# Performance work log

Hardware: AMD Instinct MI355X
Metric: run time of the kernel (lower is better)

## Reference

```python
import jax, jax.numpy as jnp
import numpy as np

NUM = 8          # group_heads
ALPHA = 1000.0   # Pos_Enc alpha
BETA = 100.0     # Pos_Enc beta


def setup_inputs() -> dict:
    key = jax.random.key(0)
    ks = jax.random.split(key, 19)
    N, C, H = 16384, 64, 1024
    gs1 = H // NUM
    s = 0.02
    r = lambda k, shp: jax.random.normal(k, shp, dtype=jnp.float32) * s
    return {
        "features": jax.random.normal(ks[0], (N, C), dtype=jnp.float32),
        "fc1_w": r(ks[1], (C, H)), "fc1_b": r(ks[2], (H,)),
        "fc2_w": r(ks[3], (H, C)), "fc2_b": r(ks[4], (C,)),
        "g1_w": r(ks[5], (H, H)), "g1_b": r(ks[6], (H,)),
        "g2_w": r(ks[7], (H, H)), "g2_b": r(ks[8], (H,)),
        "gg1_w": r(ks[9], (gs1, gs1)), "gg1_b": r(ks[10], (gs1,)),
        "gg2_w": r(ks[11], (gs1, gs1)), "gg2_b": r(ks[12], (gs1,)),
        "wq": r(ks[13], (H, H)), "wk": r(ks[14], (H, H)), "wv": r(ks[15], (H, H)),
        "wq2": r(ks[16], (gs1, gs1)), "wk2": r(ks[17], (gs1, gs1)),
        "lpe": jax.random.normal(ks[18], (1,), dtype=jnp.float32) * 0.1,
    }


def _mlp(x, w1, b1, w2, b2):
    return jax.nn.relu(x @ w1 + b1) @ w2 + b2


def reference(features, fc1_w, fc1_b, fc2_w, fc2_b, g1_w, g1_b, g2_w, g2_b,
              gg1_w, gg1_b, gg2_w, gg2_b, wq, wk, wv, wq2, wk2, lpe):
    N, C = features.shape
    H = fc1_w.shape[1]
    gs1 = H // NUM   # feature-group size
    gs2 = N // NUM   # token-group size

    x = features @ fc1_w + fc1_b                      # (N, H)

    # --- attn1: per-feature-group vector attention (shared weights -> vectorized)
    xg = x.reshape(N, NUM, gs1)                       # contiguous feature slices
    q1 = xg @ wq2
    k1 = xg @ wk2
    h1 = _mlp(q1 - k1, gg1_w, gg1_b, gg2_w, gg2_b)
    attn1 = jax.nn.softmax(h1 / np.sqrt(gs1).astype(np.float32), axis=0)
    attn1 = attn1.reshape(N, H)                       # concat over groups = reshape

    # --- attn2: source bug: loop uses stale i=NUM-1, so the LAST token group
    # is processed NUM times and tiled along tokens.
    gf2 = x[(NUM - 1) * gs2:, :]                      # (gs2, H)
    q2 = gf2 @ wq
    k2 = gf2 @ wk
    h2 = _mlp(q2 - k2, g1_w, g1_b, g2_w, g2_b)
    a2 = jax.nn.softmax(h2 / np.sqrt(H).astype(np.float32), axis=0)
    attn2 = jnp.tile(a2, (NUM, 1))                    # (N, H)

    attn = attn1 + attn2
    v = x @ wv                                        # (N, H)

    # --- sinusoidal positional encoding (Pos_Enc), only coord-0 slice survives
    xyz = features[:, :3]                             # (N, 3)
    feat_dim = H // 2
    feat_range = jnp.arange(feat_dim, dtype=jnp.float32)
    dim_embed = jnp.power(jnp.float32(ALPHA), feat_range / feat_dim)
    div = BETA * xyz[..., None] / dim_embed           # (N, 3, feat_dim)
    emb = jnp.concatenate([jnp.sin(div), jnp.cos(div)], axis=-1)  # (N, 3, H)
    pe = (emb + lpe[0]) * lpe[0]
    pe0 = pe[:, 0, :]                                 # (N, H) first coordinate

    res = attn * (v + pe0)                            # elementwise einsum bmf,bmf->bmf
    out = res @ fc2_w + fc2_b + features              # residual
    return out
```

## Files before the change

### kernel.cpp

```cpp
#include <hip/hip_runtime.h>
#include <hip/hip_bf16.h>
#include <math.h>
#include <type_traits>


typedef __attribute__((ext_vector_type(8))) short short8;
typedef __attribute__((ext_vector_type(4))) float f32x4;
typedef __attribute__((ext_vector_type(4))) float float4v;

#define GLOAD_LDS16(gptr, lptr)                                                 \
    __builtin_amdgcn_global_load_lds(                                           \
        (const __attribute__((address_space(1))) void*)(gptr),                  \
        (__attribute__((address_space(3))) void*)(lptr), 16, 0, 0)

static __device__ __forceinline__ unsigned short f2bf_bits(float v) {
    __hip_bfloat16 h = __float2bfloat16(v);
    return __builtin_bit_cast(unsigned short, h);
}
static __device__ __forceinline__ float bf_bits2f(unsigned short u) {
    return __bfloat162float(__builtin_bit_cast(__hip_bfloat16, u));
}
static __device__ __forceinline__ int swz16(int r, int c16) {
    return (r << 4) + (c16 ^ (r & 7));
}
static __device__ __forceinline__ int swz_elem(int r, int c) {
    return (r << 7) + ((((c << 1) ^ ((r & 7) << 4))) >> 1);
}
static __device__ __forceinline__ int xcd_swz(int bid, int nwg) {
    return (bid & 7) * (nwg >> 3) + (bid >> 3);
}

static __device__ void conv_t_dev(const float* __restrict__ A, const float* __restrict__ Bsub,
                                  __hip_bfloat16* __restrict__ Ot, int K, int N,
                                  int bx, int by, int tid, float* t )
{
    const int n0 = bx * 32, k0 = by * 32;
    const int tx = tid & 31, ty = tid >> 5;
    #pragma unroll
    for (int j = 0; j < 4; ++j) {
        int k = k0 + ty + j * 8;
        float v = A[(long)k * N + n0 + tx];
        if (Bsub) v -= Bsub[(long)k * N + n0 + tx];
        t[(ty + j * 8) * 33 + tx] = v;
    }
    __syncthreads();
    #pragma unroll
    for (int j = 0; j < 4; ++j) {
        int n = n0 + ty + j * 8;
        Ot[(long)n * K + k0 + tx] = __float2bfloat16(t[tx * 33 + ty + j * 8]);
    }
}

__global__ __launch_bounds__(256) void prep_k(
    const float* __restrict__ features, const float* __restrict__ fc1_w,
    const float* __restrict__ fc2_w, const float* __restrict__ fc2_b,
    const float* __restrict__ g1_w, const float* __restrict__ g2_w,
    const float* __restrict__ wq, const float* __restrict__ wk,
    const float* __restrict__ wv, const float* __restrict__ wq2,
    const float* __restrict__ wk2, const float* __restrict__ gg1_w,
    const float* __restrict__ gg2_w,
    __hip_bfloat16* __restrict__ featb, __hip_bfloat16* __restrict__ fc1T,
    __hip_bfloat16* __restrict__ fc2T, __hip_bfloat16* __restrict__ wdT,
    __hip_bfloat16* __restrict__ wvT, __hip_bfloat16* __restrict__ g1T,
    __hip_bfloat16* __restrict__ g2T, __hip_bfloat16* __restrict__ wd2T,
    __hip_bfloat16* __restrict__ gg1T, __hip_bfloat16* __restrict__ gg2T,
    float* __restrict__ invde, float* __restrict__ out)
{
    __shared__ float t[32 * 33];
    const int bid = blockIdx.x;
    const int tid = threadIdx.x;

    if (bid == 0) {
        #pragma unroll
        for (int i = 0; i < 2; ++i) {
            int idx = tid + i * 256;
            invde[idx] = exp2f(-9.96578428466209f * (float)idx * (1.f / 512.f));
        }
    } else if (bid < 257) {
        const float4v* f4 = (const float4v*)features;
        float4v* o4 = (float4v*)out;
        const float4v* b4 = (const float4v*)fc2_b;
        long base = (long)(bid - 1) * 1024;
        #pragma unroll
        for (int i = 0; i < 4; ++i) {
            long idx = base + tid + i * 256;
            o4[idx] = f4[idx] + b4[idx & 15];
        }
    } else if (bid < 769) {
        long j = (long)(bid - 257) * 256 + tid;
        const float4v* f4 = (const float4v*)features;
        float4v a = f4[j * 2], b = f4[j * 2 + 1];
        unsigned short o[8];
        #pragma unroll
        for (int q = 0; q < 4; ++q) { o[q] = f2bf_bits(a[q]); o[4 + q] = f2bf_bits(b[q]); }
        *(short8*)((unsigned short*)featb + j * 8) = *(short8*)o;
    } else if (bid < 1793) {
        int tt = bid - 769;  conv_t_dev(wq, wk, wdT, 1024, 1024, tt & 31, tt >> 5, tid, t);
    } else if (bid < 2817) {
        int tt = bid - 1793; conv_t_dev(wv, nullptr, wvT, 1024, 1024, tt & 31, tt >> 5, tid, t);
    } else if (bid < 3841) {
        int tt = bid - 2817; conv_t_dev(g1_w, nullptr, g1T, 1024, 1024, tt & 31, tt >> 5, tid, t);
    } else if (bid < 4865) {
        int tt = bid - 3841; conv_t_dev(g2_w, nullptr, g2T, 1024, 1024, tt & 31, tt >> 5, tid, t);
    } else if (bid < 4929) {
        int tt = bid - 4865; conv_t_dev(fc1_w, nullptr, fc1T, 64, 1024, tt & 31, tt >> 5, tid, t);
    } else if (bid < 4993) {
        int tt = bid - 4929; conv_t_dev(fc2_w, nullptr, fc2T, 1024, 64, tt & 1, tt >> 1, tid, t);
    } else if (bid < 5009) {
        int tt = bid - 4993; conv_t_dev(wq2, wk2, wd2T, 128, 128, tt & 3, tt >> 2, tid, t);
    } else if (bid < 5025) {
        int tt = bid - 5009; conv_t_dev(gg1_w, nullptr, gg1T, 128, 128, tt & 3, tt >> 2, tid, t);
    } else {
        int tt = bid - 5025; conv_t_dev(gg2_w, nullptr, gg2T, 128, 128, tt & 3, tt >> 2, tid, t);
    }
}

template <int OP, typename OutT>
__global__ __launch_bounds__(256) void gemm_bf16(
    const __hip_bfloat16* __restrict__ A, const __hip_bfloat16* __restrict__ Bt,
    const float* __restrict__ bias, OutT* __restrict__ Co,
    int M, int Nn, int K, float scale)
{
    __shared__ __hip_bfloat16 As[128 * 32];
    __shared__ __hip_bfloat16 Bs[128 * 32];
    const int tid = threadIdx.x;
    const int wid = tid >> 6;
    const int lane = tid & 63;
    const int nwg = gridDim.x * gridDim.y;
    const int swz = xcd_swz(blockIdx.y * gridDim.x + blockIdx.x, nwg);
    const int bm = (swz >> 3) << 7, bn = (swz & 7) << 7;
    const int wm = (wid >> 1) << 6, wn = (wid & 1) << 6;

    f32x4 acc[4][4] = {};

    const int r0 = tid >> 2, c0 = (tid & 3) << 3;
    const int r1 = (tid + 256) >> 2;
    __hip_bfloat16* lA0 = As + (size_t)(0 * 256 + (wid << 6)) * 8;
    __hip_bfloat16* lA1 = As + (size_t)(1 * 256 + (wid << 6)) * 8;
    __hip_bfloat16* lB0 = Bs + (size_t)(0 * 256 + (wid << 6)) * 8;
    __hip_bfloat16* lB1 = Bs + (size_t)(1 * 256 + (wid << 6)) * 8;

    const int arow = wm + (lane & 15);
    const int brow = wn + (lane & 15);
    const int kg = lane >> 4;

    for (int k0 = 0; k0 < K; k0 += 32) {
        GLOAD_LDS16(A + (long)(bm + r0) * K + k0 + c0, lA0);
        GLOAD_LDS16(A + (long)(bm + r1) * K + k0 + c0, lA1);
        GLOAD_LDS16(Bt + (long)(bn + r0) * K + k0 + c0, lB0);
        GLOAD_LDS16(Bt + (long)(bn + r1) * K + k0 + c0, lB1);
        __syncthreads();

        short8 af[4], bf_[4];
        #pragma unroll
        for (int m = 0; m < 4; ++m)
            af[m] = ((const short8*)As)[(arow + m * 16) * 4 + kg];
        #pragma unroll
        for (int n = 0; n < 4; ++n)
            bf_[n] = ((const short8*)Bs)[(brow + n * 16) * 4 + kg];
        #pragma unroll
        for (int m = 0; m < 4; ++m)
            #pragma unroll
            for (int n = 0; n < 4; ++n)
                acc[m][n] = __builtin_amdgcn_mfma_f32_16x16x32_bf16(
                    af[m], bf_[n], acc[m][n], 0, 0, 0);
        __syncthreads();
    }

    const int rq = (lane >> 4) << 2;
    #pragma unroll
    for (int n = 0; n < 4; ++n) {
        const int col = bn + wn + n * 16 + (lane & 15);
        const float bv = bias ? bias[col] : 0.f;
        #pragma unroll
        for (int m = 0; m < 4; ++m) {
            #pragma unroll
            for (int j = 0; j < 4; ++j) {
                const int row = bm + wm + m * 16 + rq + j;
                float cv = acc[m][n][j] + bv;
                if (OP == 1) cv = fmaxf(cv, 0.f);
                if (OP == 2) cv = __expf(cv * scale);
                if constexpr (std::is_same<OutT, float>::value)
                    Co[(long)row * Nn + col] = cv;
                else
                    Co[(long)row * Nn + col] = __float2bfloat16(cv);
            }
        }
    }
}

template <int OP, bool CS>
__global__ __launch_bounds__(256) void gemm64(
    const __hip_bfloat16* __restrict__ A, const __hip_bfloat16* __restrict__ Bt,
    const float* __restrict__ bias, __hip_bfloat16* __restrict__ Co,
    int K, float scale, float* __restrict__ pcs)
{
    __shared__ __hip_bfloat16 As[64 * 32];
    __shared__ __hip_bfloat16 Bs[128 * 32];
    const int tid = threadIdx.x;
    const int wid = tid >> 6;
    const int lane = tid & 63;
    const int nwg = gridDim.x * gridDim.y;
    const int swz = xcd_swz(blockIdx.y * gridDim.x + blockIdx.x, nwg);
    const int bm = (swz >> 3) << 6, bn = (swz & 7) << 7;
    const int wm = (wid >> 1) << 5, wn = (wid & 1) << 6;

    f32x4 acc[2][4] = {};

    const int rA = tid >> 2, c0 = (tid & 3) << 3;
    const int rB0 = tid >> 2, rB1 = (tid + 256) >> 2;
    __hip_bfloat16* lA0 = As + (size_t)(wid << 6) * 8;
    __hip_bfloat16* lB0 = Bs + (size_t)(0 * 256 + (wid << 6)) * 8;
    __hip_bfloat16* lB1 = Bs + (size_t)(1 * 256 + (wid << 6)) * 8;

    const int l15 = lane & 15;
    const int kg = lane >> 4;
    const int arow = wm + l15;
    const int brow = wn + l15;

    for (int k0 = 0; k0 < K; k0 += 32) {
        GLOAD_LDS16(A + (long)(bm + rA) * K + k0 + c0, lA0);
        GLOAD_LDS16(Bt + (long)(bn + rB0) * K + k0 + c0, lB0);
        GLOAD_LDS16(Bt + (long)(bn + rB1) * K + k0 + c0, lB1);
        __syncthreads();

        short8 af[2], bf_[4];
        #pragma unroll
        for (int m = 0; m < 2; ++m)
            af[m] = ((const short8*)As)[(arow + m * 16) * 4 + kg];
        #pragma unroll
        for (int n = 0; n < 4; ++n)
            bf_[n] = ((const short8*)Bs)[(brow + n * 16) * 4 + kg];
        #pragma unroll
        for (int m = 0; m < 2; ++m)
            #pragma unroll
            for (int n = 0; n < 4; ++n)
                acc[m][n] = __builtin_amdgcn_mfma_f32_16x16x32_bf16(
                    af[m], bf_[n], acc[m][n], 0, 0, 0);
        __syncthreads();
    }

    const int rq = (lane >> 4) << 2;
    float csum[4];
    #pragma unroll
    for (int n = 0; n < 4; ++n) {
        const int col = bn + wn + n * 16 + l15;
        const float bv = bias ? bias[col] : 0.f;
        csum[n] = 0.f;
        #pragma unroll
        for (int m = 0; m < 2; ++m) {
            #pragma unroll
            for (int j = 0; j < 4; ++j) {
                const int row = bm + wm + m * 16 + rq + j;
                float cv = acc[m][n][j] + bv;
                if (OP == 1) cv = fmaxf(cv, 0.f);
                if (OP == 2) cv = __expf(cv * scale);
                if (CS) csum[n] += cv;
                Co[(long)row * 1024 + col] = __float2bfloat16(cv);
            }
        }
    }
    if (CS) {
        __syncthreads();
        float* ps = (float*)As;
        const int slot = ((wid >> 1) << 2) | kg;
        #pragma unroll
        for (int n = 0; n < 4; ++n)
            ps[(wn + n * 16 + l15) * 8 + slot] = csum[n];
        __syncthreads();
        if (tid < 128) {
            float s = 0.f;
            #pragma unroll
            for (int q = 0; q < 8; ++q) s += ps[tid * 8 + q];
            pcs[(long)(swz >> 3) * 1024 + bn + tid] = s;
        }
    }
}

__global__ __launch_bounds__(256) void chain_k(
    const __hip_bfloat16* __restrict__ xb,
    const __hip_bfloat16* __restrict__ w1T,
    const __hip_bfloat16* __restrict__ w2T,
    const __hip_bfloat16* __restrict__ w3T,
    const float* __restrict__ b2, const float* __restrict__ b3,
    __hip_bfloat16* __restrict__ e1, float* __restrict__ pcs1)
{
    __shared__ unsigned short act[128 * 128];
    __shared__ unsigned short Wb[128 * 128];
    const int tid = threadIdx.x, wid = tid >> 6, lane = tid & 63;
    const int wm = (wid >> 1) << 6, wn = (wid & 1) << 6;
    const long tile = (long)blockIdx.x * (128 * 128);

    #pragma unroll
    for (int i = 0; i < 8; ++i) {
        int L = i * 256 + wid * 64 + lane;
        int r = L >> 4, c16o = (L & 15) ^ (r & 7);
        GLOAD_LDS16(xb + tile + r * 128 + c16o * 8,
                    (char*)act + (i * 256 + wid * 64) * 16);
        GLOAD_LDS16(w1T + r * 128 + c16o * 8,
                    (char*)Wb + (i * 256 + wid * 64) * 16);
    }
    __syncthreads();

    f32x4 acc[4][4];
    const int rq = (lane >> 4) << 2;

#define CHAIN_ZERO()                                                            \
    _Pragma("unroll") for (int m = 0; m < 4; ++m)                               \
        _Pragma("unroll") for (int n = 0; n < 4; ++n)                           \
            acc[m][n] = (f32x4){0.f, 0.f, 0.f, 0.f};

#define CHAIN_MM()                                                              \
    _Pragma("unroll") for (int ks = 0; ks < 4; ++ks) {                          \
        short8 af[4], bfv[4];                                                   \
        const int kc = ks * 4 + (lane >> 4);                                    \
        _Pragma("unroll") for (int m = 0; m < 4; ++m) {                         \
            int r = wm + m * 16 + (lane & 15);                                  \
            af[m] = *(const short8*)((const char*)act + swz16(r, kc) * 16);     \
        }                                                                       \
        _Pragma("unroll") for (int n = 0; n < 4; ++n) {                         \
            int r = wn + n * 16 + (lane & 15);                                  \
            bfv[n] = *(const short8*)((const char*)Wb + swz16(r, kc) * 16);     \
        }                                                                       \
        _Pragma("unroll") for (int m = 0; m < 4; ++m)                           \
            _Pragma("unroll") for (int n = 0; n < 4; ++n)                       \
                acc[m][n] = __builtin_amdgcn_mfma_f32_16x16x32_bf16(            \
                    af[m], bfv[n], acc[m][n], 0, 0, 0);                         \
    }

#define STAGE_W(wptr)                                                           \
    _Pragma("unroll") for (int i = 0; i < 8; ++i) {                             \
        int L = i * 256 + wid * 64 + lane;                                      \
        int r = L >> 4, c16o = (L & 15) ^ (r & 7);                              \
        GLOAD_LDS16((wptr) + r * 128 + c16o * 8,                                \
                    (char*)Wb + (i * 256 + wid * 64) * 16);                     \
    }

    CHAIN_ZERO(); CHAIN_MM();
    __syncthreads();
    STAGE_W(w2T);
    #pragma unroll
    for (int m = 0; m < 4; ++m)
        #pragma unroll
        for (int n = 0; n < 4; ++n)
            #pragma unroll
            for (int j = 0; j < 4; ++j) {
                int row = wm + m * 16 + rq + j, col = wn + n * 16 + (lane & 15);
                act[swz_elem(row, col)] = f2bf_bits(acc[m][n][j]);
            }
    __syncthreads();

    CHAIN_ZERO(); CHAIN_MM();
    __syncthreads();
    STAGE_W(w3T);
    {
        float bv[4];
        #pragma unroll
        for (int n = 0; n < 4; ++n) bv[n] = b2[wn + n * 16 + (lane & 15)];
        #pragma unroll
        for (int m = 0; m < 4; ++m)
            #pragma unroll
            for (int n = 0; n < 4; ++n)
                #pragma unroll
                for (int j = 0; j < 4; ++j) {
                    int row = wm + m * 16 + rq + j, col = wn + n * 16 + (lane & 15);
                    act[swz_elem(row, col)] = f2bf_bits(fmaxf(acc[m][n][j] + bv[n], 0.f));
                }
    }
    __syncthreads();

    CHAIN_ZERO(); CHAIN_MM();
    __syncthreads();
    {
        float bv[4];
        #pragma unroll
        for (int n = 0; n < 4; ++n) bv[n] = b3[wn + n * 16 + (lane & 15)];
        #pragma unroll
        for (int m = 0; m < 4; ++m)
            #pragma unroll
            for (int n = 0; n < 4; ++n)
                #pragma unroll
                for (int j = 0; j < 4; ++j) {
                    int row = wm + m * 16 + rq + j, col = wn + n * 16 + (lane & 15);
                    float ev = __expf((acc[m][n][j] + bv[n]) * 0.08838834764831845f);
                    act[swz_elem(row, col)] = f2bf_bits(ev);
                }
    }
    __syncthreads();

    #pragma unroll
    for (int i = 0; i < 8; ++i) {
        int idx = i * 256 + tid;
        int r = idx >> 4, c16o = idx & 15;
        short8 vd = *(const short8*)((const char*)act + swz16(r, c16o) * 16);
        *(short8*)((__hip_bfloat16*)e1 + tile + r * 128 + c16o * 8) = vd;
    }
    #pragma unroll
    for (int i = 0; i < 4; ++i) {
        int p = i * 256 + tid;
        int g = p >> 7, c = p & 127;
        float s = 0.f;
        #pragma unroll
        for (int t16 = 0; t16 < 16; ++t16) {
            int r = t16 * 8 + g;
            s += bf_bits2f(act[swz_elem(r, c)]);
        }
        pcs1[(long)blockIdx.x * 1024 + p] = s;
    }
#undef CHAIN_ZERO
#undef CHAIN_MM
#undef STAGE_W
}

__global__ void reduce_k(const float* __restrict__ pcs1, const float* __restrict__ pcs2,
                         float* __restrict__ rcs1, float* __restrict__ rcs2)
{
    __shared__ float red[16][64];
    const int tx = threadIdx.x, ty = threadIdx.y;
    if (blockIdx.x < 16) {
        const int col = blockIdx.x * 64 + tx;
        float s = 0.f;
        for (int p = ty; p < 1024; p += 16) s += pcs1[(long)p * 1024 + col];
        red[ty][tx] = s;
        __syncthreads();
        if (ty == 0) {
            float t = 0.f;
            #pragma unroll
            for (int q = 0; q < 16; ++q) t += red[q][tx];
            rcs1[col] = 1.f / t;
        }
    } else {
        const int col = (blockIdx.x - 16) * 64 + tx;
        float s = 0.f;
        for (int p = ty; p < 32; p += 16) s += pcs2[(long)p * 1024 + col];
        red[ty][tx] = s;
        __syncthreads();
        if (ty == 0) {
            float t = 0.f;
            #pragma unroll
            for (int q = 0; q < 16; ++q) t += red[q][tx];
            rcs2[col] = 1.f / t;
        }
    }
}

__global__ __launch_bounds__(256) void gemm_v_res_out(
    const __hip_bfloat16* __restrict__ A, const __hip_bfloat16* __restrict__ Bt,
    const __hip_bfloat16* __restrict__ e1, const __hip_bfloat16* __restrict__ e2,
    const float* __restrict__ rcs1, const float* __restrict__ rcs2,
    const float* __restrict__ invde, const float* __restrict__ feats,
    const float* __restrict__ lpe, const __hip_bfloat16* __restrict__ fc2T,
    float* __restrict__ out, int K)
{
    __shared__ __align__(16) char smem[34816];
    __hip_bfloat16* As = (__hip_bfloat16*)smem;
    __hip_bfloat16* Bs = (__hip_bfloat16*)(smem + 16384);
    unsigned short* st = (unsigned short*)smem;

    const int tid = threadIdx.x;
    const int wid = tid >> 6;
    const int lane = tid & 63;
    const int swz = xcd_swz(blockIdx.y * gridDim.x + blockIdx.x, gridDim.x * gridDim.y);
    const int bm = (swz >> 3) << 7, bn = (swz & 7) << 7;
    const int wm = (wid >> 1) << 6, wn = (wid & 1) << 6;

    f32x4 acc[4][4] = {};

    const int c8 = tid & 7;
    const int l15 = lane & 15;
    const int kg = lane >> 4;
    const int arow = wm + l15;
    const int brow = wn + l15;

    for (int k0 = 0; k0 < K; k0 += 64) {
        #pragma unroll
        for (int i = 0; i < 4; ++i) {
            const int r = i * 32 + (tid >> 3);
            const int c8s = c8 ^ (r & 7);
            GLOAD_LDS16(A + (long)(bm + r) * K + k0 + c8s * 8,
                        (char*)As + (i * 256 + wid * 64) * 16);
            GLOAD_LDS16(Bt + (long)(bn + r) * K + k0 + c8s * 8,
                        (char*)Bs + (i * 256 + wid * 64) * 16);
        }
        __syncthreads();

        #pragma unroll
        for (int ks2 = 0; ks2 < 2; ++ks2) {
            const int kslot = ks2 * 4 + kg;
            short8 af[4], bf_[4];
            #pragma unroll
            for (int m = 0; m < 4; ++m) {
                const int r = arow + m * 16;
                af[m] = *(const short8*)(As + (r * 8 + (kslot ^ (r & 7))) * 8);
            }
            #pragma unroll
            for (int n = 0; n < 4; ++n) {
                const int r = brow + n * 16;
                bf_[n] = *(const short8*)(Bs + (r * 8 + (kslot ^ (r & 7))) * 8);
            }
            #pragma unroll
            for (int m = 0; m < 4; ++m)
                #pragma unroll
                for (int n = 0; n < 4; ++n)
                    acc[m][n] = __builtin_amdgcn_mfma_f32_16x16x32_bf16(
                        af[m], bf_[n], acc[m][n], 0, 0, 0);
        }
        __syncthreads();
    }

    const int rq = (lane >> 4) << 2;
    #pragma unroll
    for (int m = 0; m < 4; ++m)
        #pragma unroll
        for (int n = 0; n < 4; ++n)
            #pragma unroll
            for (int j = 0; j < 4; ++j)
                st[(wm + m * 16 + rq + j) * 136 + wn + n * 16 + l15] =
                    f2bf_bits(acc[m][n][j]);
    __syncthreads();

    const float lp = lpe[0];
    #pragma unroll
    for (int p = 0; p < 4; ++p) {
        const int r = p * 32 + (tid >> 3);
        const int cc = (tid & 7) << 4;
        const int grow = bm + r;
        const float angs = 100.f * feats[(long)grow * 64];
        const long goff = (long)grow * 1024 + bn + cc;
        const long goff2 = (long)(grow & 2047) * 1024 + bn + cc;
        short8 ev1[2], ev2[2], sv[2];
        ev1[0] = *(const short8*)((const unsigned short*)e1 + goff);
        ev1[1] = *(const short8*)((const unsigned short*)e1 + goff + 8);
        ev2[0] = *(const short8*)((const unsigned short*)e2 + goff2);
        ev2[1] = *(const short8*)((const unsigned short*)e2 + goff2 + 8);
        sv[0] = *(const short8*)&st[r * 136 + cc];
        sv[1] = *(const short8*)&st[r * 136 + cc + 8];
        unsigned short ov[16];
        #pragma unroll
        for (int q = 0; q < 16; ++q) {
            const int h = bn + cc + q;
            const float ang = angs * invde[h & 511];
            const float tr = (h < 512) ? __sinf(ang) : __cosf(ang);
            const float a = bf_bits2f((unsigned short)ev1[q >> 3][q & 7]) * rcs1[h] +
                            bf_bits2f((unsigned short)ev2[q >> 3][q & 7]) * rcs2[h];
            const float vv = bf_bits2f((unsigned short)sv[q >> 3][q & 7]);
            ov[q] = f2bf_bits(a * (vv + (tr + lp) * lp));
        }
        *(short8*)&st[r * 136 + cc] = *(short8*)&ov[0];
        *(short8*)&st[r * 136 + cc + 8] = *(short8*)&ov[8];
    }
    __syncthreads();

    {
        const int wmO = wid << 5;
        f32x4 aco[2][4] = {};
        #pragma unroll
        for (int ks = 0; ks < 4; ++ks) {
            short8 afo[2], bfo[4];
            #pragma unroll
            for (int m = 0; m < 2; ++m)
                afo[m] = *(const short8*)&st[(wmO + m * 16 + l15) * 136 + ks * 32 + kg * 8];
            #pragma unroll
            for (int n = 0; n < 4; ++n)
                bfo[n] = *(const short8*)((const unsigned short*)fc2T +
                                          (long)(n * 16 + l15) * 1024 + bn + ks * 32 + kg * 8);
            #pragma unroll
            for (int m = 0; m < 2; ++m)
                #pragma unroll
                for (int n = 0; n < 4; ++n)
                    aco[m][n] = __builtin_amdgcn_mfma_f32_16x16x32_bf16(
                        afo[m], bfo[n], aco[m][n], 0, 0, 0);
        }
        #pragma unroll
        for (int m = 0; m < 2; ++m)
            #pragma unroll
            for (int n = 0; n < 4; ++n)
                #pragma unroll
                for (int j = 0; j < 4; ++j) {
                    const int row = bm + wmO + m * 16 + rq + j;
                    atomicAdd(&out[(long)row * 64 + n * 16 + l15], aco[m][n][j]);
                }
    }
}

extern "C" void kernel_launch(void* const* d_in, const int* in_sizes, int n_in,
                              void* d_out, int out_size, void* d_ws, size_t ws_size,
                              hipStream_t stream) {
    const float* features = (const float*)d_in[0];
    const float* fc1_w = (const float*)d_in[1];
    const float* fc1_b = (const float*)d_in[2];
    const float* fc2_w = (const float*)d_in[3];
    const float* fc2_b = (const float*)d_in[4];
    const float* g1_w = (const float*)d_in[5];
    const float* g1_b = (const float*)d_in[6];
    const float* g2_w = (const float*)d_in[7];
    const float* g2_b = (const float*)d_in[8];
    const float* gg1_w = (const float*)d_in[9];
    const float* gg1_b = (const float*)d_in[10];
    const float* gg2_w = (const float*)d_in[11];
    const float* gg2_b = (const float*)d_in[12];
    const float* wq = (const float*)d_in[13];
    const float* wk = (const float*)d_in[14];
    const float* wv = (const float*)d_in[15];
    const float* wq2 = (const float*)d_in[16];
    const float* wk2 = (const float*)d_in[17];
    const float* lpe = (const float*)d_in[18];
    float* out = (float*)d_out;

    char* ws = (char*)d_ws;
    const size_t MB = 1024ull * 1024ull;
    __hip_bfloat16* xb   = (__hip_bfloat16*)ws;
    __hip_bfloat16* e1   = (__hip_bfloat16*)(ws + 32 * MB);
    __hip_bfloat16* d2b  = (__hip_bfloat16*)(ws + 64 * MB);
    __hip_bfloat16* t2b  = (__hip_bfloat16*)(ws + 68 * MB);
    __hip_bfloat16* e2b  = (__hip_bfloat16*)(ws + 72 * MB);
    float*          pcs1 = (float*)(ws + 76 * MB);
    float*          pcs2 = (float*)(ws + 80 * MB);
    char* W = ws + 81 * MB;
    __hip_bfloat16* featb = (__hip_bfloat16*)W;
    __hip_bfloat16* fc1T  = (__hip_bfloat16*)(W + 2 * MB);
    __hip_bfloat16* wdT   = (__hip_bfloat16*)(W + 3 * MB);
    __hip_bfloat16* wvT   = (__hip_bfloat16*)(W + 5 * MB);
    __hip_bfloat16* g1T   = (__hip_bfloat16*)(W + 7 * MB);
    __hip_bfloat16* g2T   = (__hip_bfloat16*)(W + 9 * MB);
    __hip_bfloat16* fc2T  = (__hip_bfloat16*)(W + 11 * MB);
    __hip_bfloat16* wd2T  = (__hip_bfloat16*)(W + 12 * MB);
    __hip_bfloat16* gg1T  = (__hip_bfloat16*)(W + 12 * MB + 64 * 1024);
    __hip_bfloat16* gg2T  = (__hip_bfloat16*)(W + 12 * MB + 128 * 1024);
    float* rcs1  = (float*)(W + 13 * MB);
    float* rcs2  = rcs1 + 1024;
    float* invde = rcs2 + 1024;

    prep_k<<<5041, 256, 0, stream>>>(
        features, fc1_w, fc2_w, fc2_b, g1_w, g2_w, wq, wk, wv, wq2, wk2,
        gg1_w, gg2_w, featb, fc1T, fc2T, wdT, wvT, g1T, g2T, wd2T, gg1T, gg2T,
        invde, out);

    gemm_bf16<0, __hip_bfloat16><<<dim3(8, 128), 256, 0, stream>>>(
        featb, fc1T, fc1_b, xb, 16384, 1024, 64, 0.f);

    chain_k<<<1024, 256, 0, stream>>>(xb, wd2T, gg1T, gg2T, gg1_b, gg2_b, e1, pcs1);

    gemm64<0, false><<<dim3(8, 32), 256, 0, stream>>>(
        xb + (size_t)14336 * 1024, wdT, nullptr, d2b, 1024, 0.f, nullptr);
    gemm64<1, false><<<dim3(8, 32), 256, 0, stream>>>(
        d2b, g1T, g1_b, t2b, 1024, 0.f, nullptr);
    gemm64<2, true><<<dim3(8, 32), 256, 0, stream>>>(
        t2b, g2T, g2_b, e2b, 1024, 0.03125f, pcs2);

    reduce_k<<<32, dim3(64, 16), 0, stream>>>(pcs1, pcs2, rcs1, rcs2);

    gemm_v_res_out<<<dim3(8, 128), 256, 0, stream>>>(
        xb, wvT, e1, e2b, rcs1, rcs2, invde, features, lpe, fc2T, out, 1024);
}
```

Baseline: 309.8 us.

## Fuse fc1 GEMM into prep, merge chain with first gemm64, double-buffer GEMM loads

The fc1 projection now runs directly from fp32 features and weights inside the prep kernel, which drops the separate bf16 conversion blocks and the standalone gemm_bf16 launch. The first attn2 projection GEMM and the attn1 chain kernel are merged into one launch, so the small GEMM's blocks run alongside the chain tiles. The gemm64 and final v/out GEMM loops now double-buffer their LDS staging with explicit vmcnt waits, barriers and setprio to overlap loads with MFMA work. In exchange, LDS use per block rises to 64KB, which may lower occupancy, and the larger merged kernels carry more branch divergence across blocks.

New measurement: 297.8 us. 3.9% less time.

```diff
diff --git a/kernel.cpp b/kernel.cpp
--- a/kernel.cpp
+++ b/kernel.cpp
@@ -51,22 +51,96 @@
     }
 }
 
-__global__ __launch_bounds__(256) void prep_k(
+static __device__ void xgemm_dev(const float* __restrict__ features,
+                                 const float* __restrict__ fc1_w,
+                                 const float* __restrict__ fc1_b,
+                                 __hip_bfloat16* __restrict__ xb,
+                                 int tile, int tid, char* smem)
+{
+    unsigned short* As = (unsigned short*)smem;
+    unsigned short* Bs = (unsigned short*)(smem + 16384);
+    const int bm = (tile >> 3) << 7, bn = (tile & 7) << 7;
+    const int wid = tid >> 6, lane = tid & 63;
+    const int wm = (wid >> 1) << 6, wn = (wid & 1) << 6;
+    const int l15 = lane & 15, kg = lane >> 4;
+
+    #pragma unroll
+    for (int i = 0; i < 8; ++i) {
+        int idx = i * 256 + tid;
+        int r = idx >> 4, c4 = idx & 15;
+        float4v f = *(const float4v*)(features + (long)(bm + r) * 64 + c4 * 4);
+        unsigned int p0 = f2bf_bits(f[0]) | ((unsigned int)f2bf_bits(f[1]) << 16);
+        unsigned int p1 = f2bf_bits(f[2]) | ((unsigned int)f2bf_bits(f[3]) << 16);
+        int dst = r * 64 + (((c4 >> 1) ^ (r & 7)) << 3) + (c4 & 1) * 4;
+        unsigned int* p = (unsigned int*)&As[dst];
+        p[0] = p0; p[1] = p1;
+    }
+    #pragma unroll
+    for (int i = 0; i < 8; ++i) {
+        int idx = i * 256 + tid;
+        int k = idx >> 5, c4b = idx & 31;
+        float4v g = *(const float4v*)(fc1_w + (long)k * 1024 + bn + c4b * 4);
+        #pragma unroll
+        for (int q = 0; q < 4; ++q) {
+            int n = c4b * 4 + q;
+            Bs[n * 64 + (((k >> 3) ^ (n & 7)) << 3) + (k & 7)] = f2bf_bits(g[q]);
+        }
+    }
+    __syncthreads();
+
+    f32x4 acc[4][4] = {};
+    #pragma unroll
+    for (int ks2 = 0; ks2 < 2; ++ks2) {
+        const int kslot = ks2 * 4 + kg;
+        short8 af[4], bf_[4];
+        #pragma unroll
+        for (int m = 0; m < 4; ++m) {
+            int r = wm + m * 16 + l15;
+            af[m] = *(const short8*)&As[r * 64 + ((kslot ^ (r & 7)) << 3)];
+        }
+        #pragma unroll
+        for (int n = 0; n < 4; ++n) {
+            int r = wn + n * 16 + l15;
+            bf_[n] = *(const short8*)&Bs[r * 64 + ((kslot ^ (r & 7)) << 3)];
+        }
+        #pragma unroll
+        for (int m = 0; m < 4; ++m)
+            #pragma unroll
+            for (int n = 0; n < 4; ++n)
+                acc[m][n] = __builtin_amdgcn_mfma_f32_16x16x32_bf16(
+                    af[m], bf_[n], acc[m][n], 0, 0, 0);
+    }
+    const int rq = kg << 2;
+    #pragma unroll
+    for (int n = 0; n < 4; ++n) {
+        const int col = bn + wn + n * 16 + l15;
+        const float bv = fc1_b[col];
+        #pragma unroll
+        for (int m = 0; m < 4; ++m)
+            #pragma unroll
+            for (int j = 0; j < 4; ++j)
+                xb[(long)(bm + wm + m * 16 + rq + j) * 1024 + col] =
+                    __float2bfloat16(acc[m][n][j] + bv);
+    }
+}
+
+__global__ __launch_bounds__(256) void prep_x_k(
     const float* __restrict__ features, const float* __restrict__ fc1_w,
-    const float* __restrict__ fc2_w, const float* __restrict__ fc2_b,
-    const float* __restrict__ g1_w, const float* __restrict__ g2_w,
-    const float* __restrict__ wq, const float* __restrict__ wk,
-    const float* __restrict__ wv, const float* __restrict__ wq2,
-    const float* __restrict__ wk2, const float* __restrict__ gg1_w,
-    const float* __restrict__ gg2_w,
-    __hip_bfloat16* __restrict__ featb, __hip_bfloat16* __restrict__ fc1T,
+    const float* __restrict__ fc1_b, const float* __restrict__ fc2_w,
+    const float* __restrict__ fc2_b, const float* __restrict__ g1_w,
+    const float* __restrict__ g2_w, const float* __restrict__ wq,
+    const float* __restrict__ wk, const float* __restrict__ wv,
+    const float* __restrict__ wq2, const float* __restrict__ wk2,
+    const float* __restrict__ gg1_w, const float* __restrict__ gg2_w,
     __hip_bfloat16* __restrict__ fc2T, __hip_bfloat16* __restrict__ wdT,
     __hip_bfloat16* __restrict__ wvT, __hip_bfloat16* __restrict__ g1T,
     __hip_bfloat16* __restrict__ g2T, __hip_bfloat16* __restrict__ wd2T,
     __hip_bfloat16* __restrict__ gg1T, __hip_bfloat16* __restrict__ gg2T,
-    float* __restrict__ invde, float* __restrict__ out)
-{
-    __shared__ float t[32 * 33];
+    __hip_bfloat16* __restrict__ xb, float* __restrict__ invde,
+    float* __restrict__ out)
+{
+    __shared__ __align__(16) char smem[32768];
+    float* t = (float*)smem;
     const int bid = blockIdx.x;
     const int tid = threadIdx.x;
 
@@ -86,161 +160,83 @@
             long idx = base + tid + i * 256;
             o4[idx] = f4[idx] + b4[idx & 15];
         }
-    } else if (bid < 769) {
-        long j = (long)(bid - 257) * 256 + tid;
-        const float4v* f4 = (const float4v*)features;
-        float4v a = f4[j * 2], b = f4[j * 2 + 1];
-        unsigned short o[8];
-        #pragma unroll
-        for (int q = 0; q < 4; ++q) { o[q] = f2bf_bits(a[q]); o[4 + q] = f2bf_bits(b[q]); }
-        *(short8*)((unsigned short*)featb + j * 8) = *(short8*)o;
-    } else if (bid < 1793) {
-        int tt = bid - 769;  conv_t_dev(wq, wk, wdT, 1024, 1024, tt & 31, tt >> 5, tid, t);
-    } else if (bid < 2817) {
-        int tt = bid - 1793; conv_t_dev(wv, nullptr, wvT, 1024, 1024, tt & 31, tt >> 5, tid, t);
-    } else if (bid < 3841) {
-        int tt = bid - 2817; conv_t_dev(g1_w, nullptr, g1T, 1024, 1024, tt & 31, tt >> 5, tid, t);
-    } else if (bid < 4865) {
-        int tt = bid - 3841; conv_t_dev(g2_w, nullptr, g2T, 1024, 1024, tt & 31, tt >> 5, tid, t);
-    } else if (bid < 4929) {
-        int tt = bid - 4865; conv_t_dev(fc1_w, nullptr, fc1T, 64, 1024, tt & 31, tt >> 5, tid, t);
-    } else if (bid < 4993) {
-        int tt = bid - 4929; conv_t_dev(fc2_w, nullptr, fc2T, 1024, 64, tt & 1, tt >> 1, tid, t);
-    } else if (bid < 5009) {
-        int tt = bid - 4993; conv_t_dev(wq2, wk2, wd2T, 128, 128, tt & 3, tt >> 2, tid, t);
-    } else if (bid < 5025) {
-        int tt = bid - 5009; conv_t_dev(gg1_w, nullptr, gg1T, 128, 128, tt & 3, tt >> 2, tid, t);
+    } else if (bid < 1281) {
+        int tt = bid - 257;  conv_t_dev(wq, wk, wdT, 1024, 1024, tt & 31, tt >> 5, tid, t);
+    } else if (bid < 2305) {
+        int tt = bid - 1281; conv_t_dev(wv, nullptr, wvT, 1024, 1024, tt & 31, tt >> 5, tid, t);
+    } else if (bid < 3329) {
+        int tt = bid - 2305; conv_t_dev(g1_w, nullptr, g1T, 1024, 1024, tt & 31, tt >> 5, tid, t);
+    } else if (bid < 4353) {
+        int tt = bid - 3329; conv_t_dev(g2_w, nullptr, g2T, 1024, 1024, tt & 31, tt >> 5, tid, t);
+    } else if (bid < 4417) {
+        int tt = bid - 4353; conv_t_dev(fc2_w, nullptr, fc2T, 1024, 64, tt & 1, tt >> 1, tid, t);
+    } else if (bid < 4433) {
+        int tt = bid - 4417; conv_t_dev(wq2, wk2, wd2T, 128, 128, tt & 3, tt >> 2, tid, t);
+    } else if (bid < 4449) {
+        int tt = bid - 4433; conv_t_dev(gg1_w, nullptr, gg1T, 128, 128, tt & 3, tt >> 2, tid, t);
+    } else if (bid < 4465) {
+        int tt = bid - 4449; conv_t_dev(gg2_w, nullptr, gg2T, 128, 128, tt & 3, tt >> 2, tid, t);
     } else {
-        int tt = bid - 5025; conv_t_dev(gg2_w, nullptr, gg2T, 128, 128, tt & 3, tt >> 2, tid, t);
-    }
-}
-
-template <int OP, typename OutT>
-__global__ __launch_bounds__(256) void gemm_bf16(
+        xgemm_dev(features, fc1_w, fc1_b, xb, bid - 4465, tid, smem);
+    }
+}
+
+template <int OP, bool CS>
+static __device__ void gemm64_dev(
     const __hip_bfloat16* __restrict__ A, const __hip_bfloat16* __restrict__ Bt,
-    const float* __restrict__ bias, OutT* __restrict__ Co,
-    int M, int Nn, int K, float scale)
-{
-    __shared__ __hip_bfloat16 As[128 * 32];
-    __shared__ __hip_bfloat16 Bs[128 * 32];
-    const int tid = threadIdx.x;
-    const int wid = tid >> 6;
-    const int lane = tid & 63;
-    const int nwg = gridDim.x * gridDim.y;
-    const int swz = xcd_swz(blockIdx.y * gridDim.x + blockIdx.x, nwg);
-    const int bm = (swz >> 3) << 7, bn = (swz & 7) << 7;
-    const int wm = (wid >> 1) << 6, wn = (wid & 1) << 6;
-
-    f32x4 acc[4][4] = {};
-
-    const int r0 = tid >> 2, c0 = (tid & 3) << 3;
-    const int r1 = (tid + 256) >> 2;
-    __hip_bfloat16* lA0 = As + (size_t)(0 * 256 + (wid << 6)) * 8;
-    __hip_bfloat16* lA1 = As + (size_t)(1 * 256 + (wid << 6)) * 8;
-    __hip_bfloat16* lB0 = Bs + (size_t)(0 * 256 + (wid << 6)) * 8;
-    __hip_bfloat16* lB1 = Bs + (size_t)(1 * 256 + (wid << 6)) * 8;
-
-    const int arow = wm + (lane & 15);
-    const int brow = wn + (lane & 15);
-    const int kg = lane >> 4;
-
-    for (int k0 = 0; k0 < K; k0 += 32) {
-        GLOAD_LDS16(A + (long)(bm + r0) * K + k0 + c0, lA0);
-        GLOAD_LDS16(A + (long)(bm + r1) * K + k0 + c0, lA1);
-        GLOAD_LDS16(Bt + (long)(bn + r0) * K + k0 + c0, lB0);
-        GLOAD_LDS16(Bt + (long)(bn + r1) * K + k0 + c0, lB1);
-        __syncthreads();
-
-        short8 af[4], bf_[4];
-        #pragma unroll
-        for (int m = 0; m < 4; ++m)
+    const float* __restrict__ bias, __hip_bfloat16* __restrict__ Co,
+    float scale, float* __restrict__ pcs, int swz, int tid, char* smem)
+{
+    const int wid = tid >> 6, lane = tid & 63;
+    const int bm = (swz >> 3) << 6, bn = (swz & 7) << 7;
+    const int wm = (wid >> 1) << 5, wn = (wid & 1) << 6;
+    f32x4 acc[2][4] = {};
+    const int rA = tid >> 2, c0 = (tid & 3) << 3;
+    const int rB1 = (tid + 256) >> 2;
+    const int l15 = lane & 15, kg = lane >> 4;
+    const int arow = wm + l15, brow = wn + l15;
+
+#define G64_STAGE(b, k0)                                                        \
+    { char* base = smem + (b) * 12288;                                          \
+      GLOAD_LDS16(A + (long)(bm + rA) * 1024 + (k0) + c0, base + (wid << 6) * 16); \
+      GLOAD_LDS16(Bt + (long)(bn + rA) * 1024 + (k0) + c0,                      \
+                  base + 4096 + (wid << 6) * 16);                               \
+      GLOAD_LDS16(Bt + (long)(bn + rB1) * 1024 + (k0) + c0,                     \
+                  base + 4096 + (256 + (wid << 6)) * 16); }
+
+    G64_STAGE(0, 0);
+    #pragma unroll 2
+    for (int kt = 0; kt < 32; ++kt) {
+        if (kt < 31) {
+            G64_STAGE((kt + 1) & 1, (kt + 1) * 32);
+            asm volatile("s_waitcnt vmcnt(3)" ::: "memory");
+        } else {
+            asm volatile("s_waitcnt vmcnt(0)" ::: "memory");
+        }
+        __builtin_amdgcn_s_barrier();
+        __builtin_amdgcn_sched_barrier(0);
+        const __hip_bfloat16* As = (const __hip_bfloat16*)(smem + (kt & 1) * 12288);
+        const __hip_bfloat16* Bs = (const __hip_bfloat16*)(smem + (kt & 1) * 12288 + 4096);
+        short8 af[2], bf_[4];
+        #pragma unroll
+        for (int m = 0; m < 2; ++m)
             af[m] = ((const short8*)As)[(arow + m * 16) * 4 + kg];
         #pragma unroll
         for (int n = 0; n < 4; ++n)
             bf_[n] = ((const short8*)Bs)[(brow + n * 16) * 4 + kg];
-        #pragma unroll
-        for (int m = 0; m < 4; ++m)
+        __builtin_amdgcn_s_setprio(1);
+        #pragma unroll
+        for (int m = 0; m < 2; ++m)
             #pragma unroll
             for (int n = 0; n < 4; ++n)
                 acc[m][n] = __builtin_amdgcn_mfma_f32_16x16x32_bf16(
                     af[m], bf_[n], acc[m][n], 0, 0, 0);
-        __syncthreads();
-    }
-
-    const int rq = (lane >> 4) << 2;
-    #pragma unroll
-    for (int n = 0; n < 4; ++n) {
-        const int col = bn + wn + n * 16 + (lane & 15);
-        const float bv = bias ? bias[col] : 0.f;
-        #pragma unroll
-        for (int m = 0; m < 4; ++m) {
-            #pragma unroll
-            for (int j = 0; j < 4; ++j) {
-                const int row = bm + wm + m * 16 + rq + j;
-                float cv = acc[m][n][j] + bv;
-                if (OP == 1) cv = fmaxf(cv, 0.f);
-                if (OP == 2) cv = __expf(cv * scale);
-                if constexpr (std::is_same<OutT, float>::value)
-                    Co[(long)row * Nn + col] = cv;
-                else
-                    Co[(long)row * Nn + col] = __float2bfloat16(cv);
-            }
-        }
-    }
-}
-
-template <int OP, bool CS>
-__global__ __launch_bounds__(256) void gemm64(
-    const __hip_bfloat16* __restrict__ A, const __hip_bfloat16* __restrict__ Bt,
-    const float* __restrict__ bias, __hip_bfloat16* __restrict__ Co,
-    int K, float scale, float* __restrict__ pcs)
-{
-    __shared__ __hip_bfloat16 As[64 * 32];
-    __shared__ __hip_bfloat16 Bs[128 * 32];
-    const int tid = threadIdx.x;
-    const int wid = tid >> 6;
-    const int lane = tid & 63;
-    const int nwg = gridDim.x * gridDim.y;
-    const int swz = xcd_swz(blockIdx.y * gridDim.x + blockIdx.x, nwg);
-    const int bm = (swz >> 3) << 6, bn = (swz & 7) << 7;
-    const int wm = (wid >> 1) << 5, wn = (wid & 1) << 6;
-
-    f32x4 acc[2][4] = {};
-
-    const int rA = tid >> 2, c0 = (tid & 3) << 3;
-    const int rB0 = tid >> 2, rB1 = (tid + 256) >> 2;
-    __hip_bfloat16* lA0 = As + (size_t)(wid << 6) * 8;
-    __hip_bfloat16* lB0 = Bs + (size_t)(0 * 256 + (wid << 6)) * 8;
-    __hip_bfloat16* lB1 = Bs + (size_t)(1 * 256 + (wid << 6)) * 8;
-
-    const int l15 = lane & 15;
-    const int kg = lane >> 4;
-    const int arow = wm + l15;
-    const int brow = wn + l15;
-
-    for (int k0 = 0; k0 < K; k0 += 32) {
-        GLOAD_LDS16(A + (long)(bm + rA) * K + k0 + c0, lA0);
-        GLOAD_LDS16(Bt + (long)(bn + rB0) * K + k0 + c0, lB0);
-        GLOAD_LDS16(Bt + (long)(bn + rB1) * K + k0 + c0, lB1);
-        __syncthreads();
-
-        short8 af[2], bf_[4];
-        #pragma unroll
-        for (int m = 0; m < 2; ++m)
-            af[m] = ((const short8*)As)[(arow + m * 16) * 4 + kg];
-        #pragma unroll
-        for (int n = 0; n < 4; ++n)
-            bf_[n] = ((const short8*)Bs)[(brow + n * 16) * 4 + kg];
-        #pragma unroll
-        for (int m = 0; m < 2; ++m)
-            #pragma unroll
-            for (int n = 0; n < 4; ++n)
-                acc[m][n] = __builtin_amdgcn_mfma_f32_16x16x32_bf16(
-                    af[m], bf_[n], acc[m][n], 0, 0, 0);
-        __syncthreads();
-    }
-
-    const int rq = (lane >> 4) << 2;
+        __builtin_amdgcn_s_setprio(0);
+        __builtin_amdgcn_s_barrier();
+    }
+#undef G64_STAGE
+
+    const int rq = kg << 2;
     float csum[4];
     #pragma unroll
     for (int n = 0; n < 4; ++n) {
@@ -262,7 +258,7 @@
     }
     if (CS) {
         __syncthreads();
-        float* ps = (float*)As;
+        float* ps = (float*)smem;
         const int slot = ((wid >> 1) << 2) | kg;
         #pragma unroll
         for (int n = 0; n < 4; ++n)
@@ -277,19 +273,31 @@
     }
 }
 
-__global__ __launch_bounds__(256) void chain_k(
+template <int OP, bool CS>
+__global__ __launch_bounds__(256) void gemm64_k(
+    const __hip_bfloat16* __restrict__ A, const __hip_bfloat16* __restrict__ Bt,
+    const float* __restrict__ bias, __hip_bfloat16* __restrict__ Co,
+    float scale, float* __restrict__ pcs)
+{
+    __shared__ __align__(16) char smem[24576];
+    const int swz = xcd_swz(blockIdx.y * gridDim.x + blockIdx.x, gridDim.x * gridDim.y);
+    gemm64_dev<OP, CS>(A, Bt, bias, Co, scale, pcs, swz, threadIdx.x, smem);
+}
+
+static __device__ void chain_dev(
     const __hip_bfloat16* __restrict__ xb,
     const __hip_bfloat16* __restrict__ w1T,
     const __hip_bfloat16* __restrict__ w2T,
     const __hip_bfloat16* __restrict__ w3T,
     const float* __restrict__ b2, const float* __restrict__ b3,
-    __hip_bfloat16* __restrict__ e1, float* __restrict__ pcs1)
-{
-    __shared__ unsigned short act[128 * 128];
-    __shared__ unsigned short Wb[128 * 128];
-    const int tid = threadIdx.x, wid = tid >> 6, lane = tid & 63;
+    __hip_bfloat16* __restrict__ e1, float* __restrict__ pcs1,
+    int tileIdx, int tid, char* smem)
+{
+    unsigned short* act = (unsigned short*)smem;
+    unsigned short* Wb  = (unsigned short*)(smem + 32768);
+    const int wid = tid >> 6, lane = tid & 63;
     const int wm = (wid >> 1) << 6, wn = (wid & 1) << 6;
-    const long tile = (long)blockIdx.x * (128 * 128);
+    const long tile = (long)tileIdx * (128 * 128);
 
     #pragma unroll
     for (int i = 0; i < 8; ++i) {
@@ -405,15 +413,34 @@
             int r = t16 * 8 + g;
             s += bf_bits2f(act[swz_elem(r, c)]);
         }
-        pcs1[(long)blockIdx.x * 1024 + p] = s;
+        pcs1[(long)tileIdx * 1024 + p] = s;
     }
 #undef CHAIN_ZERO
 #undef CHAIN_MM
 #undef STAGE_W
 }
 
-__global__ void reduce_k(const float* __restrict__ pcs1, const float* __restrict__ pcs2,
-                         float* __restrict__ rcs1, float* __restrict__ rcs2)
+__global__ __launch_bounds__(256) void mid_k(
+    const __hip_bfloat16* __restrict__ xb, const __hip_bfloat16* __restrict__ wdT,
+    __hip_bfloat16* __restrict__ d2b,
+    const __hip_bfloat16* __restrict__ wd2T, const __hip_bfloat16* __restrict__ gg1T,
+    const __hip_bfloat16* __restrict__ gg2T, const float* __restrict__ gg1_b,
+    const float* __restrict__ gg2_b, __hip_bfloat16* __restrict__ e1,
+    float* __restrict__ pcs1)
+{
+    __shared__ __align__(16) char smem[65536];
+    const int bid = blockIdx.x, tid = threadIdx.x;
+    if (bid < 256) {
+        gemm64_dev<0, false>(xb + (size_t)14336 * 1024, wdT, nullptr, d2b,
+                             0.f, nullptr, xcd_swz(bid, 256), tid, smem);
+    } else {
+        chain_dev(xb, wd2T, gg1T, gg2T, gg1_b, gg2_b, e1, pcs1, bid - 256, tid, smem);
+    }
+}
+
+__global__ __launch_bounds__(1024) void reduce_k(
+    const float* __restrict__ pcs1, const float* __restrict__ pcs2,
+    float* __restrict__ rcs1, float* __restrict__ rcs2)
 {
     __shared__ float red[16][64];
     const int tx = threadIdx.x, ty = threadIdx.y;
@@ -450,11 +477,9 @@
     const float* __restrict__ rcs1, const float* __restrict__ rcs2,
     const float* __restrict__ invde, const float* __restrict__ feats,
     const float* __restrict__ lpe, const __hip_bfloat16* __restrict__ fc2T,
-    float* __restrict__ out, int K)
-{
-    __shared__ __align__(16) char smem[34816];
-    __hip_bfloat16* As = (__hip_bfloat16*)smem;
-    __hip_bfloat16* Bs = (__hip_bfloat16*)(smem + 16384);
+    float* __restrict__ out)
+{
+    __shared__ __align__(16) char smem[65536];
     unsigned short* st = (unsigned short*)smem;
 
     const int tid = threadIdx.x;
@@ -465,25 +490,36 @@
     const int wm = (wid >> 1) << 6, wn = (wid & 1) << 6;
 
     f32x4 acc[4][4] = {};
-
     const int c8 = tid & 7;
     const int l15 = lane & 15;
     const int kg = lane >> 4;
     const int arow = wm + l15;
     const int brow = wn + l15;
 
-    for (int k0 = 0; k0 < K; k0 += 64) {
-        #pragma unroll
-        for (int i = 0; i < 4; ++i) {
-            const int r = i * 32 + (tid >> 3);
-            const int c8s = c8 ^ (r & 7);
-            GLOAD_LDS16(A + (long)(bm + r) * K + k0 + c8s * 8,
-                        (char*)As + (i * 256 + wid * 64) * 16);
-            GLOAD_LDS16(Bt + (long)(bn + r) * K + k0 + c8s * 8,
-                        (char*)Bs + (i * 256 + wid * 64) * 16);
-        }
-        __syncthreads();
-
+#define VR_STAGE(b, k0)                                                         \
+    { char* base = smem + (b) * 32768;                                          \
+      _Pragma("unroll") for (int i = 0; i < 4; ++i) {                           \
+        const int r = i * 32 + (tid >> 3);                                      \
+        const int c8s = c8 ^ (r & 7);                                           \
+        GLOAD_LDS16(A + (long)(bm + r) * 1024 + (k0) + c8s * 8,                 \
+                    base + (i * 256 + wid * 64) * 16);                          \
+        GLOAD_LDS16(Bt + (long)(bn + r) * 1024 + (k0) + c8s * 8,                \
+                    base + 16384 + (i * 256 + wid * 64) * 16); } }
+
+    VR_STAGE(0, 0);
+    #pragma unroll 2
+    for (int kt = 0; kt < 16; ++kt) {
+        if (kt < 15) {
+            VR_STAGE((kt + 1) & 1, (kt + 1) * 64);
+            asm volatile("s_waitcnt vmcnt(8)" ::: "memory");
+        } else {
+            asm volatile("s_waitcnt vmcnt(0)" ::: "memory");
+        }
+        __builtin_amdgcn_s_barrier();
+        __builtin_amdgcn_sched_barrier(0);
+        const __hip_bfloat16* As = (const __hip_bfloat16*)(smem + (kt & 1) * 32768);
+        const __hip_bfloat16* Bs = (const __hip_bfloat16*)(smem + (kt & 1) * 32768 + 16384);
+        __builtin_amdgcn_s_setprio(1);
         #pragma unroll
         for (int ks2 = 0; ks2 < 2; ++ks2) {
             const int kslot = ks2 * 4 + kg;
@@ -505,10 +541,12 @@
                     acc[m][n] = __builtin_amdgcn_mfma_f32_16x16x32_bf16(
                         af[m], bf_[n], acc[m][n], 0, 0, 0);
         }
-        __syncthreads();
-    }
-
-    const int rq = (lane >> 4) << 2;
+        __builtin_amdgcn_s_setprio(0);
+        __builtin_amdgcn_s_barrier();
+    }
+#undef VR_STAGE
+
+    const int rq = kg << 2;
     #pragma unroll
     for (int m = 0; m < 4; ++m)
         #pragma unroll
@@ -617,39 +655,30 @@
     float*          pcs1 = (float*)(ws + 76 * MB);
     float*          pcs2 = (float*)(ws + 80 * MB);
     char* W = ws + 81 * MB;
-    __hip_bfloat16* featb = (__hip_bfloat16*)W;
-    __hip_bfloat16* fc1T  = (__hip_bfloat16*)(W + 2 * MB);
-    __hip_bfloat16* wdT   = (__hip_bfloat16*)(W + 3 * MB);
-    __hip_bfloat16* wvT   = (__hip_bfloat16*)(W + 5 * MB);
-    __hip_bfloat16* g1T   = (__hip_bfloat16*)(W + 7 * MB);
-    __hip_bfloat16* g2T   = (__hip_bfloat16*)(W + 9 * MB);
-    __hip_bfloat16* fc2T  = (__hip_bfloat16*)(W + 11 * MB);
-    __hip_bfloat16* wd2T  = (__hip_bfloat16*)(W + 12 * MB);
-    __hip_bfloat16* gg1T  = (__hip_bfloat16*)(W + 12 * MB + 64 * 1024);
-    __hip_bfloat16* gg2T  = (__hip_bfloat16*)(W + 12 * MB + 128 * 1024);
-    float* rcs1  = (float*)(W + 13 * MB);
+    __hip_bfloat16* wdT   = (__hip_bfloat16*)W;
+    __hip_bfloat16* wvT   = (__hip_bfloat16*)(W + 2 * MB);
+    __hip_bfloat16* g1T   = (__hip_bfloat16*)(W + 4 * MB);
+    __hip_bfloat16* g2T   = (__hip_bfloat16*)(W + 6 * MB);
+    __hip_bfloat16* fc2T  = (__hip_bfloat16*)(W + 8 * MB);
+    __hip_bfloat16* wd2T  = (__hip_bfloat16*)(W + 8 * MB + 256 * 1024);
+    __hip_bfloat16* gg1T  = (__hip_bfloat16*)(W + 8 * MB + 320 * 1024);
+    __hip_bfloat16* gg2T  = (__hip_bfloat16*)(W + 8 * MB + 384 * 1024);
+    float* rcs1  = (float*)(W + 9 * MB);
     float* rcs2  = rcs1 + 1024;
     float* invde = rcs2 + 1024;
 
-    prep_k<<<5041, 256, 0, stream>>>(
-        features, fc1_w, fc2_w, fc2_b, g1_w, g2_w, wq, wk, wv, wq2, wk2,
-        gg1_w, gg2_w, featb, fc1T, fc2T, wdT, wvT, g1T, g2T, wd2T, gg1T, gg2T,
-        invde, out);
-
-    gemm_bf16<0, __hip_bfloat16><<<dim3(8, 128), 256, 0, stream>>>(
-        featb, fc1T, fc1_b, xb, 16384, 1024, 64, 0.f);
-
-    chain_k<<<1024, 256, 0, stream>>>(xb, wd2T, gg1T, gg2T, gg1_b, gg2_b, e1, pcs1);
-
-    gemm64<0, false><<<dim3(8, 32), 256, 0, stream>>>(
-        xb + (size_t)14336 * 1024, wdT, nullptr, d2b, 1024, 0.f, nullptr);
-    gemm64<1, false><<<dim3(8, 32), 256, 0, stream>>>(
-        d2b, g1T, g1_b, t2b, 1024, 0.f, nullptr);
-    gemm64<2, true><<<dim3(8, 32), 256, 0, stream>>>(
-        t2b, g2T, g2_b, e2b, 1024, 0.03125f, pcs2);
+    prep_x_k<<<5489, 256, 0, stream>>>(
+        features, fc1_w, fc1_b, fc2_w, fc2_b, g1_w, g2_w, wq, wk, wv, wq2, wk2,
+        gg1_w, gg2_w, fc2T, wdT, wvT, g1T, g2T, wd2T, gg1T, gg2T, xb, invde, out);
+
+    mid_k<<<1280, 256, 0, stream>>>(xb, wdT, d2b, wd2T, gg1T, gg2T,
+                                    gg1_b, gg2_b, e1, pcs1);
+
+    gemm64_k<1, false><<<dim3(8, 32), 256, 0, stream>>>(d2b, g1T, g1_b, t2b, 0.f, nullptr);
+    gemm64_k<2, true><<<dim3(8, 32), 256, 0, stream>>>(t2b, g2T, g2_b, e2b, 0.03125f, pcs2);
 
     reduce_k<<<32, dim3(64, 16), 0, stream>>>(pcs1, pcs2, rcs1, rcs2);
 
     gemm_v_res_out<<<dim3(8, 128), 256, 0, stream>>>(
-        xb, wvT, e1, e2b, rcs1, rcs2, invde, features, lpe, fc2T, out, 1024);
-}
+        xb, wvT, e1, e2b, rcs1, rcs2, invde, features, lpe, fc2T, out);
+}
```
